# Performance work log

Measured on AMD Instinct MI355X. Metric: run time of the kernel, lower is better.

Reference implementation:

```python
import jax, jax.numpy as jnp
import numpy as np

NUM_OBJ = 256
NUM_REL = 4096
OBJ_DIM = 4096
REL_DIM = 4096
HIDDEN = 512
NUM_OBJ_CLS = 151
NUM_REL_CLS = 51


def setup_inputs() -> dict:
    key = jax.random.key(0)
    ks = jax.random.split(key, 8)
    obj_fmaps = jax.random.normal(ks[0], (NUM_OBJ, OBJ_DIM), dtype=jnp.float32)
    obj_logits = jax.random.normal(ks[1], (NUM_OBJ, NUM_OBJ_CLS), dtype=jnp.float32)
    rel_inds = jax.random.randint(ks[2], (NUM_REL, 3), 0, NUM_OBJ, dtype=jnp.int64)
    vr = jax.random.normal(ks[3], (NUM_REL, REL_DIM), dtype=jnp.float32)
    # learned params (nn.Linear: y = x @ W.T + b)
    s_o = 1.0 / np.sqrt(OBJ_DIM)
    s_r = 1.0 / np.sqrt(REL_DIM)
    Wo = jax.random.uniform(ks[4], (HIDDEN, OBJ_DIM), jnp.float32, -s_o, s_o)
    bo = jax.random.uniform(ks[5], (HIDDEN,), jnp.float32, -s_o, s_o)
    Wr = jax.random.uniform(ks[6], (HIDDEN, REL_DIM), jnp.float32, -s_r, s_r)
    br = jax.random.uniform(ks[7], (HIDDEN,), jnp.float32, -s_r, s_r)
    return {"obj_fmaps": obj_fmaps, "obj_logits": obj_logits, "rel_inds": rel_inds,
            "vr": vr, "Wo": Wo, "bo": bo, "Wr": Wr, "br": br}


def reference(obj_fmaps, obj_logits, rel_inds, vr, Wo, bo, Wr, br):
    # mode == 'sgcls', training (no NMS branch), obj_labels=None
    obj_dists2 = obj_logits
    obj_preds = jnp.argmax(obj_dists2[:, 1:], axis=1) + 1  # [N_obj]

    sub = rel_inds[:, 1]
    obj = rel_inds[:, 2]
    sub_obj_preds = jnp.stack([obj_preds[sub], obj_preds[obj]], axis=1)  # [N_rel, 2]

    obj_h = obj_fmaps @ Wo.T + bo      # [N_obj, H]
    vr_h = vr @ Wr.T + br              # [N_rel, H]

    # per-relation node features: [sub_feat, obj_feat, vr repeated num_rel_cls times]
    R, H = vr_h.shape
    input_ggnn = jnp.concatenate([
        obj_h[sub][:, None, :],                                   # [R, 1, H]
        obj_h[obj][:, None, :],                                   # [R, 1, H]
        jnp.broadcast_to(vr_h[:, None, :], (R, NUM_REL_CLS, H)),  # [R, 51, H]
    ], axis=1)  # [R, 2 + num_rel_cls, H]

    return obj_dists2, obj_preds, sub_obj_preds, input_ggnn
```

## Files before the change

### kernel.cpp

```cpp
#include <hip/hip_runtime.h>

#define NUM_OBJ 256
#define NUM_REL 4096
#define OBJ_DIM 4096
#define REL_DIM 4096
#define HIDDEN 512
#define NUM_OBJ_CLS 151
#define NUM_REL_CLS 51

#define OFF_PREDS (NUM_OBJ * NUM_OBJ_CLS)
#define OFF_SOP   (OFF_PREDS + NUM_OBJ)
#define OFF_GGNN  (OFF_SOP + NUM_REL * 2)

#define M_TOT (NUM_OBJ + NUM_REL)
#define KDIM  4096

typedef __attribute__((ext_vector_type(4))) float          f32x4;
typedef __attribute__((ext_vector_type(8))) short          bf16x8;
typedef __attribute__((ext_vector_type(4))) unsigned short u16x4;

__device__ __forceinline__ unsigned short f2bf(float f) {
  unsigned int u = __float_as_uint(f);
  u += 0x7FFFu + ((u >> 16) & 1u);
  return (unsigned short)(u >> 16);
}

__device__ __forceinline__ void gload16(const short* g, short* l) {
  __builtin_amdgcn_global_load_lds(
      (const __attribute__((address_space(1))) unsigned int*)g,
      (__attribute__((address_space(3))) unsigned int*)l, 16, 0, 0);
}

__global__ __launch_bounds__(64) void preds_kernel(const float* __restrict__ logits,
                                                   float* __restrict__ out) {
  const int row = blockIdx.x;
  const int lane = threadIdx.x;
  const float* lrow = logits + row * NUM_OBJ_CLS;
  float best = -3.0e38f;
  int bidx = NUM_OBJ_CLS;
  for (int j = lane; j < NUM_OBJ_CLS; j += 64) {
    float v = lrow[j];
    out[row * NUM_OBJ_CLS + j] = v;
    if (j >= 1 && v > best) { best = v; bidx = j; }
  }
  for (int off = 1; off < 64; off <<= 1) {
    float ob = __shfl_xor(best, off);
    int   oi = __shfl_xor(bidx, off);
    if (ob > best || (ob == best && oi < bidx)) { best = ob; bidx = oi; }
  }
  if (lane == 0) out[OFF_PREDS + row] = (float)bidx;
}

__global__ __launch_bounds__(256) void convert_kernel(const float* __restrict__ obj_fmaps,
                                                      const float* __restrict__ vr,
                                                      const float* __restrict__ Wo,
                                                      const float* __restrict__ Wr,
                                                      short* __restrict__ A_bf,
                                                      short* __restrict__ W_bf) {
  const int NA = M_TOT * (KDIM / 4);
  const int NW = 1024 * (KDIM / 4);
  for (int i = blockIdx.x * 256 + threadIdx.x; i < NA + NW; i += gridDim.x * 256) {
    const float* src;
    short* dst;
    if (i < NA) {
      int row = i >> 10, c = i & 1023;
      src = (row < NUM_OBJ ? obj_fmaps + ((size_t)row << 12)
                           : vr + ((size_t)(row - NUM_OBJ) << 12)) + c * 4;
      dst = A_bf + ((size_t)row << 12) + c * 4;
    } else {
      int j = i - NA;
      int row = j >> 10, c = j & 1023;
      src = (row < HIDDEN ? Wo + ((size_t)row << 12)
                          : Wr + ((size_t)(row - HIDDEN) << 12)) + c * 4;
      dst = W_bf + ((size_t)row << 12) + c * 4;
    }
    f32x4 v = *(const f32x4*)src;
    u16x4 h = {f2bf(v.x), f2bf(v.y), f2bf(v.z), f2bf(v.w)};
    *(u16x4*)dst = h;
  }
}

#define GBK 64
#define GNKT (KDIM / GBK)

__global__ __launch_bounds__(256) void gemm_bf16(const short* __restrict__ A_bf,
                                                 const short* __restrict__ W_bf,
                                                 const float* __restrict__ bo,
                                                 const float* __restrict__ br,
                                                 float* __restrict__ H) {
  __shared__ short lds[2][2][64 * 64];
  const int mb = blockIdx.x, nb = blockIdx.y;
  const int m0 = mb * 64, n0 = nb * 64;
  const short* Asrc = A_bf + (size_t)m0 * KDIM;
  const short* Bsrc = W_bf + (mb < 4 ? 0 : (size_t)HIDDEN * KDIM) + (size_t)n0 * KDIM;
  const float* bias = (mb < 4) ? bo : br;

  const int t = threadIdx.x, lane = t & 63, w = t >> 6;
  const int wm = w >> 1, wn = w & 1, lr = lane & 15, kg = lane >> 4;

  int rowS[2], colS[2];
#pragma unroll
  for (int c = 0; c < 2; ++c) {
    int row = w * 16 + c * 8 + (lane >> 3);
    rowS[c] = row;
    colS[c] = ((lane & 7) * 8) ^ ((row & 7) << 3);
  }

  f32x4 acc[2][2];
#pragma unroll
  for (int i = 0; i < 2; ++i)
#pragma unroll
    for (int j = 0; j < 2; ++j) acc[i][j] = (f32x4)0.0f;

#define STAGE(buf, kt)                                                              \
  {                                                                                 \
    _Pragma("unroll")                                                               \
    for (int c = 0; c < 2; ++c) {                                                   \
      gload16(Asrc + (size_t)rowS[c] * KDIM + (kt) * GBK + colS[c],                 \
              &lds[buf][0][w * 1024 + c * 512]);                                    \
      gload16(Bsrc + (size_t)rowS[c] * KDIM + (kt) * GBK + colS[c],                 \
              &lds[buf][1][w * 1024 + c * 512]);                                    \
    }                                                                               \
  }

  STAGE(0, 0);
  __syncthreads();

  int cur = 0;
  for (int kt = 0; kt < GNKT; ++kt) {
    if (kt + 1 < GNKT) STAGE(cur ^ 1, kt + 1);

    bf16x8 a[2][2], b[2][2];
#pragma unroll
    for (int i = 0; i < 2; ++i) {
      int r = wm * 32 + i * 16 + lr;
      int sw = (r & 7) << 3;
#pragma unroll
      for (int ks = 0; ks < 2; ++ks)
        a[i][ks] = *(const bf16x8*)&lds[cur][0][r * 64 + ((ks * 32 + kg * 8) ^ sw)];
    }
#pragma unroll
    for (int j = 0; j < 2; ++j) {
      int r = wn * 32 + j * 16 + lr;
      int sw = (r & 7) << 3;
#pragma unroll
      for (int ks = 0; ks < 2; ++ks)
        b[j][ks] = *(const bf16x8*)&lds[cur][1][r * 64 + ((ks * 32 + kg * 8) ^ sw)];
    }

#pragma unroll
    for (int ks = 0; ks < 2; ++ks)
#pragma unroll
      for (int i = 0; i < 2; ++i)
#pragma unroll
        for (int j = 0; j < 2; ++j)
          acc[i][j] = __builtin_amdgcn_mfma_f32_16x16x32_bf16(a[i][ks], b[j][ks], acc[i][j], 0, 0, 0);

    __syncthreads();
    cur ^= 1;
  }

#pragma unroll
  for (int i = 0; i < 2; ++i) {
#pragma unroll
    for (int j = 0; j < 2; ++j) {
      int gcol = n0 + wn * 32 + j * 16 + lr;
      float bv = bias[gcol];
#pragma unroll
      for (int q = 0; q < 4; ++q) {
        int grow = m0 + wm * 32 + i * 16 + kg * 4 + q;
        H[(size_t)grow * HIDDEN + gcol] = acc[i][j][q] + bv;
      }
    }
  }
#undef STAGE
}

#define BM 128
#define BN 64
#define BK 32
#define LDP 40

__global__ __launch_bounds__(256) void gemm_bt_bias(const float* __restrict__ A,
                                                    const float* __restrict__ W,
                                                    const float* __restrict__ bias,
                                                    float* __restrict__ C, int K) {
  __shared__ short Al[BM * LDP];
  __shared__ short Bl[BN * LDP];
  const int t = threadIdx.x;
  const int m0 = blockIdx.x * BM;
  const int n0 = blockIdx.y * BN;
  const int lane = t & 63, wave = t >> 6;
  const int wm = wave >> 1, wn = wave & 1;
  const int lr = lane & 15, kg = lane >> 4;

  f32x4 acc[4][2];
#pragma unroll
  for (int i = 0; i < 4; ++i)
#pragma unroll
    for (int j = 0; j < 2; ++j) acc[i][j] = (f32x4)0.0f;

  const int nkt = K / BK;
  for (int kt = 0; kt < nkt; ++kt) {
#pragma unroll
    for (int s = t; s < 1536; s += 256) {
      if (s < 1024) {
        int r = s >> 3, c4 = s & 7;
        f32x4 v = *(const f32x4*)(A + (size_t)(m0 + r) * K + kt * BK + c4 * 4);
        u16x4 h = {f2bf(v.x), f2bf(v.y), f2bf(v.z), f2bf(v.w)};
        *(u16x4*)&Al[r * LDP + c4 * 4] = h;
      } else {
        int s2 = s - 1024;
        int r = s2 >> 3, c4 = s2 & 7;
        f32x4 v = *(const f32x4*)(W + (size_t)(n0 + r) * K + kt * BK + c4 * 4);
        u16x4 h = {f2bf(v.x), f2bf(v.y), f2bf(v.z), f2bf(v.w)};
        *(u16x4*)&Bl[r * LDP + c4 * 4] = h;
      }
    }
    __syncthreads();

    bf16x8 a[4], b[2];
#pragma unroll
    for (int i = 0; i < 4; ++i)
      a[i] = *(const bf16x8*)&Al[(wm * 64 + i * 16 + lr) * LDP + kg * 8];
#pragma unroll
    for (int j = 0; j < 2; ++j)
      b[j] = *(const bf16x8*)&Bl[(wn * 32 + j * 16 + lr) * LDP + kg * 8];
#pragma unroll
    for (int i = 0; i < 4; ++i)
#pragma unroll
      for (int j = 0; j < 2; ++j)
        acc[i][j] = __builtin_amdgcn_mfma_f32_16x16x32_bf16(a[i], b[j], acc[i][j], 0, 0, 0);
    __syncthreads();
  }

#pragma unroll
  for (int i = 0; i < 4; ++i) {
#pragma unroll
    for (int j = 0; j < 2; ++j) {
      int gcol = n0 + wn * 32 + j * 16 + lr;
      float bv = bias[gcol];
#pragma unroll
      for (int q = 0; q < 4; ++q) {
        int grow = m0 + wm * 64 + i * 16 + kg * 4 + q;
        C[(size_t)grow * HIDDEN + gcol] = acc[i][j][q] + bv;
      }
    }
  }
}

__global__ __launch_bounds__(256) void scatter_kernel(const int* __restrict__ rel_inds,
                                                      const float* __restrict__ obj_h,
                                                      const float* __restrict__ vr_h,
                                                      float* __restrict__ out) {
  const int r = blockIdx.x;
  const int s = rel_inds[r * 3 + 1];
  const int o = rel_inds[r * 3 + 2];
  const int t = threadIdx.x;
  if (t == 0) out[OFF_SOP + r * 2 + 0] = out[OFF_PREDS + s];
  if (t == 1) out[OFF_SOP + r * 2 + 1] = out[OFF_PREDS + o];

  const int c4 = t & 127;
  const int half = t >> 7;
  f32x4 vs = *(const f32x4*)(obj_h + (size_t)s * HIDDEN + c4 * 4);
  f32x4 vo = *(const f32x4*)(obj_h + (size_t)o * HIDDEN + c4 * 4);
  f32x4 vv = *(const f32x4*)(vr_h + (size_t)r * HIDDEN + c4 * 4);
  f32x4* o4 = (f32x4*)(out + OFF_GGNN + (size_t)r * (2 + NUM_REL_CLS) * HIDDEN);
  for (int row = half; row < 2 + NUM_REL_CLS; row += 2) {
    f32x4 val = (row == 0) ? vs : ((row == 1) ? vo : vv);
    o4[row * 128 + c4] = val;
  }
}

extern "C" void kernel_launch(void* const* d_in, const int* in_sizes, int n_in,
                              void* d_out, int out_size, void* d_ws, size_t ws_size,
                              hipStream_t stream) {
  const float* obj_fmaps  = (const float*)d_in[0];
  const float* obj_logits = (const float*)d_in[1];
  const int*   rel_inds   = (const int*)d_in[2];
  const float* vr         = (const float*)d_in[3];
  const float* Wo         = (const float*)d_in[4];
  const float* bo         = (const float*)d_in[5];
  const float* Wr         = (const float*)d_in[6];
  const float* br         = (const float*)d_in[7];
  float* out = (float*)d_out;

  const size_t H_BYTES = (size_t)M_TOT * HIDDEN * 4;
  const size_t A_BYTES = (size_t)M_TOT * KDIM * 2;
  const size_t W_BYTES = (size_t)1024 * KDIM * 2;

  preds_kernel<<<NUM_OBJ, 64, 0, stream>>>(obj_logits, out);

  if (ws_size >= H_BYTES + A_BYTES + W_BYTES) {
    float* H    = (float*)d_ws;
    float* obj_h = H;
    float* vr_h  = H + (size_t)NUM_OBJ * HIDDEN;
    short* A_bf = (short*)((char*)d_ws + H_BYTES);
    short* W_bf = (short*)((char*)d_ws + H_BYTES + A_BYTES);

    convert_kernel<<<2048, 256, 0, stream>>>(obj_fmaps, vr, Wo, Wr, A_bf, W_bf);
    gemm_bf16<<<dim3(M_TOT / 64, HIDDEN / 64), 256, 0, stream>>>(A_bf, W_bf, bo, br, H);
    scatter_kernel<<<NUM_REL, 256, 0, stream>>>(rel_inds, obj_h, vr_h, out);
  } else {
    float* obj_h = (float*)d_ws;
    float* vr_h  = obj_h + NUM_OBJ * HIDDEN;
    gemm_bt_bias<<<dim3(NUM_OBJ / BM, HIDDEN / BN), 256, 0, stream>>>(obj_fmaps, Wo, bo, obj_h, OBJ_DIM);
    gemm_bt_bias<<<dim3(NUM_REL / BM, HIDDEN / BN), 256, 0, stream>>>(vr, Wr, br, vr_h, REL_DIM);
    scatter_kernel<<<NUM_REL, 256, 0, stream>>>(rel_inds, obj_h, vr_h, out);
  }
}
```

Before: 158.1 us.

## Deepen GEMM LDS pipeline to four buffers with prefetch distance two

Replaces the double-buffered bf16 GEMM main loop with a four-slot LDS ring that issues global-to-LDS loads two k-tiles ahead. Synchronization uses explicit vmcnt waits plus s_barrier instead of __syncthreads, so one barrier per iteration covers both load completion and reuse of buffers. The aim is to hide more global-load latency behind MFMA work. In exchange LDS use doubles to 64KB per block, which may reduce occupancy, and correctness now depends on the hand-counted vmcnt values matching the number of loads issued per stage.

```diff
diff --git a/kernel.cpp b/kernel.cpp
--- a/kernel.cpp
+++ b/kernel.cpp
@@ -88,7 +88,7 @@
                                                  const float* __restrict__ bo,
                                                  const float* __restrict__ br,
                                                  float* __restrict__ H) {
-  __shared__ short lds[2][2][64 * 64];
+  __shared__ short lds[4][2][64 * 64];
   const int mb = blockIdx.x, nb = blockIdx.y;
   const int m0 = mb * 64, n0 = nb * 64;
   const short* Asrc = A_bf + (size_t)m0 * KDIM;
@@ -123,42 +123,51 @@
     }                                                                               \
   }
 
+#define COMPUTE(buf)                                                                \
+  {                                                                                 \
+    bf16x8 a[2][2], b[2][2];                                                        \
+    _Pragma("unroll")                                                               \
+    for (int i = 0; i < 2; ++i) {                                                   \
+      int r = wm * 32 + i * 16 + lr;                                                \
+      int sw = (r & 7) << 3;                                                        \
+      _Pragma("unroll")                                                             \
+      for (int ks = 0; ks < 2; ++ks)                                                \
+        a[i][ks] = *(const bf16x8*)&lds[buf][0][r * 64 + ((ks * 32 + kg * 8) ^ sw)];\
+    }                                                                               \
+    _Pragma("unroll")                                                               \
+    for (int j = 0; j < 2; ++j) {                                                   \
+      int r = wn * 32 + j * 16 + lr;                                                \
+      int sw = (r & 7) << 3;                                                        \
+      _Pragma("unroll")                                                             \
+      for (int ks = 0; ks < 2; ++ks)                                                \
+        b[j][ks] = *(const bf16x8*)&lds[buf][1][r * 64 + ((ks * 32 + kg * 8) ^ sw)];\
+    }                                                                               \
+    _Pragma("unroll")                                                               \
+    for (int ks = 0; ks < 2; ++ks)                                                  \
+      _Pragma("unroll")                                                             \
+      for (int i = 0; i < 2; ++i)                                                   \
+        _Pragma("unroll")                                                           \
+        for (int j = 0; j < 2; ++j)                                                 \
+          acc[i][j] =                                                               \
+              __builtin_amdgcn_mfma_f32_16x16x32_bf16(a[i][ks], b[j][ks], acc[i][j], 0, 0, 0); \
+  }
+
   STAGE(0, 0);
-  __syncthreads();
-
-  int cur = 0;
-  for (int kt = 0; kt < GNKT; ++kt) {
-    if (kt + 1 < GNKT) STAGE(cur ^ 1, kt + 1);
-
-    bf16x8 a[2][2], b[2][2];
-#pragma unroll
-    for (int i = 0; i < 2; ++i) {
-      int r = wm * 32 + i * 16 + lr;
-      int sw = (r & 7) << 3;
-#pragma unroll
-      for (int ks = 0; ks < 2; ++ks)
-        a[i][ks] = *(const bf16x8*)&lds[cur][0][r * 64 + ((ks * 32 + kg * 8) ^ sw)];
-    }
-#pragma unroll
-    for (int j = 0; j < 2; ++j) {
-      int r = wn * 32 + j * 16 + lr;
-      int sw = (r & 7) << 3;
-#pragma unroll
-      for (int ks = 0; ks < 2; ++ks)
-        b[j][ks] = *(const bf16x8*)&lds[cur][1][r * 64 + ((ks * 32 + kg * 8) ^ sw)];
-    }
-
-#pragma unroll
-    for (int ks = 0; ks < 2; ++ks)
-#pragma unroll
-      for (int i = 0; i < 2; ++i)
-#pragma unroll
-        for (int j = 0; j < 2; ++j)
-          acc[i][j] = __builtin_amdgcn_mfma_f32_16x16x32_bf16(a[i][ks], b[j][ks], acc[i][j], 0, 0, 0);
-
-    __syncthreads();
-    cur ^= 1;
-  }
+  STAGE(1, 1);
+
+  for (int kt = 0; kt < GNKT - 2; ++kt) {
+    STAGE((kt + 2) & 3, kt + 2);
+    __builtin_amdgcn_sched_barrier(0);
+    asm volatile("s_waitcnt vmcnt(8)" ::: "memory");
+    asm volatile("s_barrier" ::: "memory");
+    COMPUTE(kt & 3);
+  }
+  asm volatile("s_waitcnt vmcnt(4)" ::: "memory");
+  asm volatile("s_barrier" ::: "memory");
+  COMPUTE((GNKT - 2) & 3);
+  asm volatile("s_waitcnt vmcnt(0)" ::: "memory");
+  asm volatile("s_barrier" ::: "memory");
+  COMPUTE((GNKT - 1) & 3);
 
 #pragma unroll
   for (int i = 0; i < 2; ++i) {
@@ -174,6 +183,7 @@
     }
   }
 #undef STAGE
+#undef COMPUTE
 }
 
 #define BM 128
```

Measured after the change: 165.4 us. +4.6%, slower.
